# Optimization experiments

Measured on AMD Instinct MI355X. Metric: run time of the kernel, lower is better.

## Reference

```python
import jax, jax.numpy as jnp
import numpy as np

B, N, CIN, COUT, P = 16, 10000, 8, 32, 8
E = 160000
TRAIN_OR_PREDICT = 1


def setup_inputs() -> dict:
    key = jax.random.key(0)
    ks = jax.random.split(key, 12)
    inp = {}
    inp["X"] = jax.random.normal(ks[0], (B, N, CIN, 2 * P), dtype=jnp.float32)
    inp["edge_index"] = jax.random.randint(ks[1], (2, E), 0, N, dtype=jnp.int64)
    inp["edge_weight"] = jax.random.uniform(ks[2], (E,), dtype=jnp.float32)
    inp["attention"] = jax.random.uniform(ks[3], (2 * P,), dtype=jnp.float32)
    sc = 1.0 / np.sqrt(CIN)
    sl = 1.0 / np.sqrt(2 * COUT)
    names = ["z", "r", "h"]
    for i, g in enumerate(names):
        inp["Wc" + g] = jax.random.normal(ks[4 + i], (CIN, COUT), dtype=jnp.float32) * sc
        inp["bc" + g] = jnp.zeros((COUT,), dtype=jnp.float32)
        inp["Wl" + g] = jax.random.normal(ks[7 + i], (2 * COUT, COUT), dtype=jnp.float32) * sl
        inp["bl" + g] = jnp.zeros((COUT,), dtype=jnp.float32)
    return inp


def _gcn_norm(edge_index, edge_weight, n):
    # PyG gcn_norm: add self-loops (weight 1.0), symmetric D^-1/2 (A+I) D^-1/2
    src, dst = edge_index[0], edge_index[1]
    loop = jnp.arange(n)
    src = jnp.concatenate([src, loop])
    dst = jnp.concatenate([dst, loop])
    w = jnp.concatenate([edge_weight, jnp.ones((n,), edge_weight.dtype)])
    deg = jax.ops.segment_sum(w, dst, num_segments=n)
    dinv = jnp.where(deg > 0, deg ** -0.5, 0.0)
    return src, dst, dinv[src] * w * dinv[dst]


def _gcn(X, W, b, src, dst, norm, n):
    # propagate-then-transform: (A_hat X) W + b  (linear, identical to X W then A_hat)
    msg = X[:, src, :] * norm[None, :, None]                     # (B, E', Cin)
    agg = jax.ops.segment_sum(jnp.swapaxes(msg, 0, 1), dst, num_segments=n)  # (N, B, Cin)
    return jnp.einsum('bni,io->bno', jnp.swapaxes(agg, 0, 1), W) + b


def reference(X, edge_index, edge_weight, attention,
              Wcz, bcz, Wlz, blz, Wcr, bcr, Wlr, blr, Wch, bch, Wlh, blh):
    b_, n, _, t2 = X.shape
    p = t2 // 2
    src, dst, norm = _gcn_norm(edge_index, edge_weight, n)
    probs = jax.nn.softmax(attention)
    # backward half of the sum is scaled by TrainorPredict (linearity of the weighted sum)
    ws = jnp.concatenate([probs[:p], probs[p:] * TRAIN_OR_PREDICT])
    H0 = jnp.zeros((b_, n, Wlz.shape[1]), X.dtype)
    Xs = jnp.moveaxis(X, 3, 0)  # (2P, B, N, Cin); H is never chained in the original loop

    def cell(x):
        Z = jax.nn.sigmoid(jnp.concatenate([_gcn(x, Wcz, bcz, src, dst, norm, n), H0], -1) @ Wlz + blz)
        R = jax.nn.sigmoid(jnp.concatenate([_gcn(x, Wcr, bcr, src, dst, norm, n), H0], -1) @ Wlr + blr)
        Ht = jnp.tanh(jnp.concatenate([_gcn(x, Wch, bch, src, dst, norm, n), H0 * R], -1) @ Wlh + blh)
        return Z * H0 + (1.0 - Z) * Ht

    def step(acc, pw):
        x, w = pw
        return acc + w * cell(x), None

    out, _ = jax.lax.scan(step, H0, (Xs, ws))
    return out
```

## Files before the change

### kernel.cpp

```cpp
#include <hip/hip_runtime.h>
#include <stdint.h>

#define NN 10000
#define NE 160000
#define NB 16
#define NT 8

typedef __attribute__((ext_vector_type(8))) float f32x8;
typedef __attribute__((ext_vector_type(4))) float f32x4;
typedef __attribute__((ext_vector_type(2))) float f32x2;
typedef __attribute__((ext_vector_type(8))) _Float16 h16x8;

#define AGG_LD 136

__device__ __forceinline__ int ei_stride(const int* __restrict__ ei) {
    int z = ei[1] | ei[3] | ei[5] | ei[7] | ei[9] | ei[11] | ei[13] | ei[15];
    return (z == 0) ? 2 : 1;
}

__global__ void k_zero(float* deg, int* count) {
    int i = blockIdx.x * blockDim.x + threadIdx.x;
    if (i < NN) { deg[i] = 0.f; count[i] = 0; }
}

__global__ __launch_bounds__(256)
void k_repack(const float* __restrict__ X, h16x8* __restrict__ X2,
              float* dz, int* cz) {
    int gid = blockIdx.x * blockDim.x + threadIdx.x;
    int gsz = gridDim.x * blockDim.x;
    for (int i = gid; i < NN; i += gsz) { dz[i] = 0.f; cz[i] = 0; }
    const int total = NN * 256;
    for (int i = gid; i < total; i += gsz) {
        int n = i >> 8, t = i & 255;
        int b = t >> 4, chunk = t & 15;
        f32x8 w = ((const f32x8*)X)[((size_t)b * NN + n) * 16 + chunk];
        h16x8 h;
        #pragma unroll
        for (int j = 0; j < 8; ++j) h[j] = (_Float16)w[j];
        X2[((size_t)(b >> 1) * NN + n) * 32 + (b & 1) * 16 + chunk] = h;
    }
}

__global__ void k_degree(const int* __restrict__ ei, const float* __restrict__ ew,
                         float* deg, int* count) {
    int e = blockIdx.x * blockDim.x + threadIdx.x;
    if (e >= NE) return;
    int stride = ei_stride(ei);
    int d = ei[(size_t)(NE + e) * stride];
    atomicAdd(&deg[d], ew[e]);
    atomicAdd(&count[d], 1);
}

__global__ void k_scan_consts(const float* __restrict__ deg, const int* __restrict__ count,
                              float* dinv, int* offsets, int* fillptr,
                              const float* __restrict__ attn,
                              const float* __restrict__ Wcz, const float* __restrict__ bcz,
                              const float* __restrict__ Wlz, const float* __restrict__ blz,
                              const float* __restrict__ Wch, const float* __restrict__ bch,
                              const float* __restrict__ Wlh, const float* __restrict__ blh,
                              float* consts) {
    int tid = threadIdx.x;
    if (blockIdx.x == 1) {
        if (tid < 256) {
            int c = tid >> 5, o = tid & 31;
            float mz = 0.f, mh = 0.f;
            for (int k = 0; k < 32; ++k) {
                mz += Wcz[c * 32 + k] * Wlz[k * 32 + o];
                mh += Wch[c * 32 + k] * Wlh[k * 32 + o];
            }
            consts[tid] = mz;
            consts[256 + tid] = mh;
        }
        if (tid < 32) {
            float cz = blz[tid], ch = blh[tid];
            for (int k = 0; k < 32; ++k) {
                cz += bcz[k] * Wlz[k * 32 + tid];
                ch += bch[k] * Wlh[k * 32 + tid];
            }
            consts[512 + tid] = cz;
            consts[544 + tid] = ch;
        }
        if (tid == 0) {
            float a[16], m = -1e30f, s = 0.f;
            for (int t = 0; t < 16; ++t) { a[t] = attn[t]; m = fmaxf(m, a[t]); }
            for (int t = 0; t < 16; ++t) { a[t] = __expf(a[t] - m); s += a[t]; }
            for (int t = 0; t < 16; ++t) consts[576 + t] = a[t] / s;
        }
        return;
    }
    int lane = tid & 63, wv = tid >> 6;
    __shared__ int wsum[16];
    __shared__ int carry;
    if (tid == 0) carry = 0;
    __syncthreads();
    for (int base = 0; base < NN; base += 1024) {
        int i = base + tid;
        int v = (i < NN) ? count[i] : 0;
        int x = v;
        #pragma unroll
        for (int s = 1; s < 64; s <<= 1) {
            int y = __shfl_up(x, s, 64);
            if (lane >= s) x += y;
        }
        if (lane == 63) wsum[wv] = x;
        __syncthreads();
        if (wv == 0 && lane < 16) {
            int y = wsum[lane];
            #pragma unroll
            for (int s = 1; s < 16; s <<= 1) {
                int z = __shfl_up(y, s, 64);
                if (lane >= s) y += z;
            }
            wsum[lane] = y;
        }
        __syncthreads();
        int wbase = (wv == 0) ? 0 : wsum[wv - 1];
        int incl = carry + wbase + x;
        int excl = incl - v;
        if (i < NN) { offsets[i] = excl; fillptr[i] = excl; }
        __syncthreads();
        if (tid == 1023) carry = incl;
        __syncthreads();
    }
    for (int i = tid; i < NN; i += 1024) dinv[i] = rsqrtf(deg[i] + 1.0f);
}

__global__ void k_fill(const int* __restrict__ ei, const float* __restrict__ ew,
                       const float* __restrict__ dinv,
                       int* fillptr, int* csr_src, float* csr_norm) {
    int e = blockIdx.x * blockDim.x + threadIdx.x;
    if (e >= NE) return;
    int stride = ei_stride(ei);
    int s = ei[(size_t)e * stride];
    int d = ei[(size_t)(NE + e) * stride];
    int pos = atomicAdd(&fillptr[d], 1);
    csr_src[pos] = s;
    csr_norm[pos] = dinv[s] * ew[e] * dinv[d];
}

__device__ __forceinline__ float gatefn(float uz, float uh) {
    float ez = __expf(uz);
    float eh = __expf(2.f * uh);
    return (eh - 1.f) * __builtin_amdgcn_rcpf((1.f + ez) * (eh + 1.f));
}

__global__ __launch_bounds__(256)
void k_main_h(const h16x8* __restrict__ X2,
              const int* __restrict__ offsets, const int* __restrict__ count,
              const float* __restrict__ dinv,
              const int* __restrict__ csr_src, const float* __restrict__ csr_norm,
              const float* __restrict__ consts,
              float* __restrict__ out) {
    __shared__ float sAgg[2 * NT * AGG_LD];
    __shared__ float sMz[256], sMh[256], sCz[32], sCh[32], sWs[16];
    int tid = threadIdx.x;
    int bp   = blockIdx.x & 7;
    int tile = blockIdx.x >> 3;

    sMz[tid] = consts[tid];
    sMh[tid] = consts[256 + tid];
    if (tid < 32) { sCz[tid] = consts[512 + tid]; sCh[tid] = consts[544 + tid]; }
    if (tid < 16) sWs[tid] = consts[576 + tid];

    int ns = tid >> 5;
    int lane = tid & 31;
    int n = tile * NT + ns;
    const h16x8* xb = X2 + ((size_t)bp * NN) * 32;
    float dn = dinv[n];
    float selfn = dn * dn;
    float acc[8];
    {
        h16x8 w = xb[(size_t)n * 32 + lane];
        #pragma unroll
        for (int j = 0; j < 8; ++j) acc[j] = selfn * (float)w[j];
    }
    int off = offsets[n], cnt = count[n];
    const int*   sp  = csr_src + off;
    const float* npv = csr_norm + off;
    int e = 0;
    if (cnt >= 8) {
        int s0 = sp[0], s1 = sp[1], s2 = sp[2], s3 = sp[3];
        h16x8 a0 = xb[(size_t)s0 * 32 + lane];
        h16x8 a1 = xb[(size_t)s1 * 32 + lane];
        h16x8 a2 = xb[(size_t)s2 * 32 + lane];
        h16x8 a3 = xb[(size_t)s3 * 32 + lane];
        for (e = 4; e + 4 <= cnt; e += 4) {
            int t0 = sp[e], t1 = sp[e + 1], t2 = sp[e + 2], t3 = sp[e + 3];
            h16x8 b0 = xb[(size_t)t0 * 32 + lane];
            h16x8 b1 = xb[(size_t)t1 * 32 + lane];
            h16x8 b2 = xb[(size_t)t2 * 32 + lane];
            h16x8 b3 = xb[(size_t)t3 * 32 + lane];
            __builtin_amdgcn_sched_barrier(0);
            float n0 = npv[e - 4], n1 = npv[e - 3], n2 = npv[e - 2], n3 = npv[e - 1];
            #pragma unroll
            for (int j = 0; j < 8; ++j) acc[j] += n0 * (float)a0[j];
            #pragma unroll
            for (int j = 0; j < 8; ++j) acc[j] += n1 * (float)a1[j];
            #pragma unroll
            for (int j = 0; j < 8; ++j) acc[j] += n2 * (float)a2[j];
            #pragma unroll
            for (int j = 0; j < 8; ++j) acc[j] += n3 * (float)a3[j];
            a0 = b0; a1 = b1; a2 = b2; a3 = b3;
        }
        float n0 = npv[e - 4], n1 = npv[e - 3], n2 = npv[e - 2], n3 = npv[e - 1];
        #pragma unroll
        for (int j = 0; j < 8; ++j) acc[j] += n0 * (float)a0[j];
        #pragma unroll
        for (int j = 0; j < 8; ++j) acc[j] += n1 * (float)a1[j];
        #pragma unroll
        for (int j = 0; j < 8; ++j) acc[j] += n2 * (float)a2[j];
        #pragma unroll
        for (int j = 0; j < 8; ++j) acc[j] += n3 * (float)a3[j];
    }
    for (; e < cnt; ++e) {
        int s = sp[e];
        float nrm = npv[e];
        h16x8 w = xb[(size_t)s * 32 + lane];
        #pragma unroll
        for (int j = 0; j < 8; ++j) acc[j] += nrm * (float)w[j];
    }
    {
        int half = lane >> 4;
        int chunk = lane & 15;
        int r = ns * 2 + half;
        int c = chunk >> 1;
        int tpb = (chunk & 1) * 4;
        float* rowp = &sAgg[r * AGG_LD + c * 2];
        #pragma unroll
        for (int k = 0; k < 4; ++k) {
            f32x2 v = {acc[2 * k], acc[2 * k + 1]};
            *(f32x2*)&rowp[(tpb + k) * 16] = v;
        }
    }
    __syncthreads();

    int o = tid & 31, ns2 = tid >> 5;
    int n2 = tile * NT + ns2;
    float mz[8], mh[8];
    #pragma unroll
    for (int c = 0; c < 8; ++c) { mz[c] = sMz[c * 32 + o]; mh[c] = sMh[c * 32 + o]; }
    float czo = sCz[o], cho = sCh[o];
    const f32x4* r0 = (const f32x4*)&sAgg[(ns2 * 2 + 0) * AGG_LD];
    const f32x4* r1 = (const f32x4*)&sAgg[(ns2 * 2 + 1) * AGG_LD];
    f32x2 out0 = {0.f, 0.f}, out1 = {0.f, 0.f};
    #pragma unroll
    for (int tp = 0; tp < 8; ++tp) {
        f32x4 A0[4], A1[4];
        #pragma unroll
        for (int k = 0; k < 4; ++k) { A0[k] = r0[tp * 4 + k]; A1[k] = r1[tp * 4 + k]; }
        f32x2 uz0 = {czo, czo}, uh0 = {cho, cho};
        f32x2 uz1 = {czo, czo}, uh1 = {cho, cho};
        #pragma unroll
        for (int k = 0; k < 4; ++k) {
            f32x2 p0 = A0[k].xy, q0 = A0[k].zw;
            f32x2 p1 = A1[k].xy, q1 = A1[k].zw;
            float m0 = mz[2 * k], m1 = mz[2 * k + 1];
            float v0 = mh[2 * k], v1 = mh[2 * k + 1];
            uz0 += p0 * m0; uz0 += q0 * m1;
            uh0 += p0 * v0; uh0 += q0 * v1;
            uz1 += p1 * m0; uz1 += q1 * m1;
            uh1 += p1 * v0; uh1 += q1 * v1;
        }
        f32x2 wsp = {sWs[2 * tp], sWs[2 * tp + 1]};
        f32x2 g0, g1;
        g0.x = gatefn(uz0.x, uh0.x); g0.y = gatefn(uz0.y, uh0.y);
        g1.x = gatefn(uz1.x, uh1.x); g1.y = gatefn(uz1.y, uh1.y);
        out0 += wsp * g0;
        out1 += wsp * g1;
    }
    out[((size_t)(bp * 2 + 0) * NN + n2) * 32 + o] = out0.x + out0.y;
    out[((size_t)(bp * 2 + 1) * NN + n2) * 32 + o] = out1.x + out1.y;
}

__global__ __launch_bounds__(256)
void k_main_f32(const float* __restrict__ X,
                const int* __restrict__ offsets, const int* __restrict__ count,
                const float* __restrict__ dinv,
                const int* __restrict__ csr_src, const float* __restrict__ csr_norm,
                const float* __restrict__ consts,
                float* __restrict__ out) {
    __shared__ float sAgg[NB * 128];
    __shared__ float sMz[256], sMh[256], sCz[32], sCh[32], sWs[16];
    int tid = threadIdx.x;
    int n = blockIdx.x;

    sMz[tid] = consts[tid];
    sMh[tid] = consts[256 + tid];
    if (tid < 32) { sCz[tid] = consts[512 + tid]; sCh[tid] = consts[544 + tid]; }
    if (tid < 16) sWs[tid] = consts[576 + tid];

    int b = tid >> 4, chunk = tid & 15;
    const f32x8* xv = (const f32x8*)X;
    float dn = dinv[n];
    float selfn = dn * dn;
    float acc[8];
    {
        f32x8 w = xv[((size_t)b * NN + n) * 16 + chunk];
        #pragma unroll
        for (int j = 0; j < 8; ++j) acc[j] = selfn * w[j];
    }
    int off = offsets[n], cnt = count[n];
    for (int e = off; e < off + cnt; ++e) {
        int s = csr_src[e];
        float nrm = csr_norm[e];
        f32x8 w = xv[((size_t)b * NN + s) * 16 + chunk];
        #pragma unroll
        for (int j = 0; j < 8; ++j) acc[j] += nrm * w[j];
    }
    #pragma unroll
    for (int j = 0; j < 8; ++j) sAgg[tid * 8 + j] = acc[j];
    __syncthreads();

    int o = tid & 31, b0 = tid >> 5;
    float mz[8], mh[8];
    #pragma unroll
    for (int c = 0; c < 8; ++c) { mz[c] = sMz[c * 32 + o]; mh[c] = sMh[c * 32 + o]; }
    float czo = sCz[o], cho = sCh[o];
    float acc0 = 0.f, acc1 = 0.f;
    #pragma unroll
    for (int t = 0; t < 16; ++t) {
        float uz0 = czo, uh0 = cho, uz1 = czo, uh1 = cho;
        #pragma unroll
        for (int c = 0; c < 8; ++c) {
            float a0 = sAgg[b0 * 128 + c * 16 + t];
            float a1 = sAgg[(b0 + 8) * 128 + c * 16 + t];
            uz0 += a0 * mz[c]; uh0 += a0 * mh[c];
            uz1 += a1 * mz[c]; uh1 += a1 * mh[c];
        }
        float w = sWs[t];
        acc0 += w * gatefn(uz0, uh0);
        acc1 += w * gatefn(uz1, uh1);
    }
    out[((size_t)b0 * NN + n) * 32 + o]       = acc0;
    out[((size_t)(b0 + 8) * NN + n) * 32 + o] = acc1;
}

extern "C" void kernel_launch(void* const* d_in, const int* in_sizes, int n_in,
                              void* d_out, int out_size, void* d_ws, size_t ws_size,
                              hipStream_t stream) {
    const float* X    = (const float*)d_in[0];
    const int*   ei   = (const int*)d_in[1];
    const float* ew   = (const float*)d_in[2];
    const float* attn = (const float*)d_in[3];
    const float* Wcz  = (const float*)d_in[4];
    const float* bcz  = (const float*)d_in[5];
    const float* Wlz  = (const float*)d_in[6];
    const float* blz  = (const float*)d_in[7];
    const float* Wch  = (const float*)d_in[12];
    const float* bch  = (const float*)d_in[13];
    const float* Wlh  = (const float*)d_in[14];
    const float* blh  = (const float*)d_in[15];
    float* out = (float*)d_out;

    const size_t x2_bytes = (size_t)NN * 256 * 16;
    const size_t small_bytes = (size_t)NN * 4 * 5 + (size_t)NE * 4 * 2 + 592 * 4;
    bool use_h = (ws_size >= x2_bytes + small_bytes);

    char* p = (char*)d_ws;
    h16x8* X2 = nullptr;
    if (use_h) { X2 = (h16x8*)p; p += x2_bytes; }
    float* deg      = (float*)p; p += NN * 4;
    float* dinv     = (float*)p; p += NN * 4;
    int*   count    = (int*)p;   p += NN * 4;
    int*   offsets  = (int*)p;   p += NN * 4;
    int*   fillptr  = (int*)p;   p += NN * 4;
    int*   csr_src  = (int*)p;   p += NE * 4;
    float* csr_norm = (float*)p; p += NE * 4;
    float* consts   = (float*)p; p += 592 * 4;

    if (use_h) {
        hipLaunchKernelGGL(k_repack, dim3(1280), dim3(256), 0, stream, X, X2, deg, count);
    } else {
        hipLaunchKernelGGL(k_zero, dim3((NN + 255) / 256), dim3(256), 0, stream, deg, count);
    }
    hipLaunchKernelGGL(k_degree, dim3((NE + 255) / 256), dim3(256), 0, stream, ei, ew, deg, count);
    hipLaunchKernelGGL(k_scan_consts, dim3(2), dim3(1024), 0, stream,
                       deg, count, dinv, offsets, fillptr,
                       attn, Wcz, bcz, Wlz, blz, Wch, bch, Wlh, blh, consts);
    hipLaunchKernelGGL(k_fill, dim3((NE + 255) / 256), dim3(256), 0, stream,
                       ei, ew, dinv, fillptr, csr_src, csr_norm);
    if (use_h) {
        hipLaunchKernelGGL(k_main_h, dim3((NN / NT) * 8), dim3(256), 0, stream,
                           X2, offsets, count, dinv, csr_src, csr_norm, consts, out);
    } else {
        hipLaunchKernelGGL(k_main_f32, dim3(NN), dim3(256), 0, stream,
                           X, offsets, count, dinv, csr_src, csr_norm, consts, out);
    }
}
```

Baseline: 155.6 us.

## Fuse prep kernels and split each node's edges across half-waves

Merges the repack, degree-count and constant-folding kernels into one grid-stride prep kernel. A memset now zeroes deg and count, which were reordered to sit next to each other, and the scan runs as its own one-block kernel. The main kernel now uses NT=4 nodes per block with one 64-lane wave per node: each half-wave gathers alternate edges, and a shuffle-xor combines the two partial sums, which doubles memory-level parallelism per node and halves the per-thread gather count. The epilogue handles one (batch,node) row per 32 threads, and the grid doubles in block count with more per-block constant loading overhead.

```diff
diff --git a/kernel.cpp b/kernel.cpp
--- a/kernel.cpp
+++ b/kernel.cpp
@@ -4,7 +4,7 @@
 #define NN 10000
 #define NE 160000
 #define NB 16
-#define NT 8
+#define NT 4
 
 typedef __attribute__((ext_vector_type(8))) float f32x8;
 typedef __attribute__((ext_vector_type(4))) float f32x4;
@@ -18,50 +18,39 @@
     return (z == 0) ? 2 : 1;
 }
 
-__global__ void k_zero(float* deg, int* count) {
-    int i = blockIdx.x * blockDim.x + threadIdx.x;
-    if (i < NN) { deg[i] = 0.f; count[i] = 0; }
-}
-
 __global__ __launch_bounds__(256)
-void k_repack(const float* __restrict__ X, h16x8* __restrict__ X2,
-              float* dz, int* cz) {
+void k_prep(const float* __restrict__ X, h16x8* __restrict__ X2, int do_repack,
+            const int* __restrict__ ei, const float* __restrict__ ew,
+            float* deg, int* count,
+            const float* __restrict__ attn,
+            const float* __restrict__ Wcz, const float* __restrict__ bcz,
+            const float* __restrict__ Wlz, const float* __restrict__ blz,
+            const float* __restrict__ Wch, const float* __restrict__ bch,
+            const float* __restrict__ Wlh, const float* __restrict__ blh,
+            float* consts) {
     int gid = blockIdx.x * blockDim.x + threadIdx.x;
     int gsz = gridDim.x * blockDim.x;
-    for (int i = gid; i < NN; i += gsz) { dz[i] = 0.f; cz[i] = 0; }
-    const int total = NN * 256;
-    for (int i = gid; i < total; i += gsz) {
-        int n = i >> 8, t = i & 255;
-        int b = t >> 4, chunk = t & 15;
-        f32x8 w = ((const f32x8*)X)[((size_t)b * NN + n) * 16 + chunk];
-        h16x8 h;
-        #pragma unroll
-        for (int j = 0; j < 8; ++j) h[j] = (_Float16)w[j];
-        X2[((size_t)(b >> 1) * NN + n) * 32 + (b & 1) * 16 + chunk] = h;
-    }
-}
-
-__global__ void k_degree(const int* __restrict__ ei, const float* __restrict__ ew,
-                         float* deg, int* count) {
-    int e = blockIdx.x * blockDim.x + threadIdx.x;
-    if (e >= NE) return;
     int stride = ei_stride(ei);
-    int d = ei[(size_t)(NE + e) * stride];
-    atomicAdd(&deg[d], ew[e]);
-    atomicAdd(&count[d], 1);
-}
-
-__global__ void k_scan_consts(const float* __restrict__ deg, const int* __restrict__ count,
-                              float* dinv, int* offsets, int* fillptr,
-                              const float* __restrict__ attn,
-                              const float* __restrict__ Wcz, const float* __restrict__ bcz,
-                              const float* __restrict__ Wlz, const float* __restrict__ blz,
-                              const float* __restrict__ Wch, const float* __restrict__ bch,
-                              const float* __restrict__ Wlh, const float* __restrict__ blh,
-                              float* consts) {
-    int tid = threadIdx.x;
-    if (blockIdx.x == 1) {
-        if (tid < 256) {
+    for (int e = gid; e < NE; e += gsz) {
+        int d = ei[(size_t)(NE + e) * stride];
+        atomicAdd(&deg[d], ew[e]);
+        atomicAdd(&count[d], 1);
+    }
+    if (do_repack) {
+        const int total = NN * 256;
+        for (int i = gid; i < total; i += gsz) {
+            int n = i >> 8, t = i & 255;
+            int b = t >> 4, chunk = t & 15;
+            f32x8 w = ((const f32x8*)X)[((size_t)b * NN + n) * 16 + chunk];
+            h16x8 h;
+            #pragma unroll
+            for (int j = 0; j < 8; ++j) h[j] = (_Float16)w[j];
+            X2[((size_t)(b >> 1) * NN + n) * 32 + (b & 1) * 16 + chunk] = h;
+        }
+    }
+    if (blockIdx.x == 0) {
+        int tid = threadIdx.x;
+        {
             int c = tid >> 5, o = tid & 31;
             float mz = 0.f, mh = 0.f;
             for (int k = 0; k < 32; ++k) {
@@ -86,8 +75,12 @@
             for (int t = 0; t < 16; ++t) { a[t] = __expf(a[t] - m); s += a[t]; }
             for (int t = 0; t < 16; ++t) consts[576 + t] = a[t] / s;
         }
-        return;
-    }
+    }
+}
+
+__global__ void k_scan(const float* __restrict__ deg, const int* __restrict__ count,
+                       float* dinv, int* offsets, int* fillptr) {
+    int tid = threadIdx.x;
     int lane = tid & 63, wv = tid >> 6;
     __shared__ int wsum[16];
     __shared__ int carry;
@@ -162,15 +155,17 @@
     if (tid < 32) { sCz[tid] = consts[512 + tid]; sCh[tid] = consts[544 + tid]; }
     if (tid < 16) sWs[tid] = consts[576 + tid];
 
-    int ns = tid >> 5;
-    int lane = tid & 31;
-    int n = tile * NT + ns;
+    int lane = tid & 63;
+    int wv = __builtin_amdgcn_readfirstlane(tid >> 6);
+    int half = lane >> 5;
+    int chunk = lane & 31;
+    int n = tile * NT + wv;
     const h16x8* xb = X2 + ((size_t)bp * NN) * 32;
     float dn = dinv[n];
-    float selfn = dn * dn;
+    float selfn = (half == 0) ? dn * dn : 0.f;
     float acc[8];
     {
-        h16x8 w = xb[(size_t)n * 32 + lane];
+        h16x8 w = xb[(size_t)n * 32 + chunk];
         #pragma unroll
         for (int j = 0; j < 8; ++j) acc[j] = selfn * (float)w[j];
     }
@@ -180,51 +175,54 @@
     int e = 0;
     if (cnt >= 8) {
         int s0 = sp[0], s1 = sp[1], s2 = sp[2], s3 = sp[3];
-        h16x8 a0 = xb[(size_t)s0 * 32 + lane];
-        h16x8 a1 = xb[(size_t)s1 * 32 + lane];
-        h16x8 a2 = xb[(size_t)s2 * 32 + lane];
-        h16x8 a3 = xb[(size_t)s3 * 32 + lane];
+        int sa = half ? s1 : s0, sb = half ? s3 : s2;
+        h16x8 a0 = xb[(size_t)sa * 32 + chunk];
+        h16x8 a1 = xb[(size_t)sb * 32 + chunk];
         for (e = 4; e + 4 <= cnt; e += 4) {
             int t0 = sp[e], t1 = sp[e + 1], t2 = sp[e + 2], t3 = sp[e + 3];
-            h16x8 b0 = xb[(size_t)t0 * 32 + lane];
-            h16x8 b1 = xb[(size_t)t1 * 32 + lane];
-            h16x8 b2 = xb[(size_t)t2 * 32 + lane];
-            h16x8 b3 = xb[(size_t)t3 * 32 + lane];
+            int ta = half ? t1 : t0, tb = half ? t3 : t2;
+            h16x8 b0 = xb[(size_t)ta * 32 + chunk];
+            h16x8 b1 = xb[(size_t)tb * 32 + chunk];
             __builtin_amdgcn_sched_barrier(0);
             float n0 = npv[e - 4], n1 = npv[e - 3], n2 = npv[e - 2], n3 = npv[e - 1];
+            float na = half ? n1 : n0, nb = half ? n3 : n2;
             #pragma unroll
-            for (int j = 0; j < 8; ++j) acc[j] += n0 * (float)a0[j];
+            for (int j = 0; j < 8; ++j) acc[j] += na * (float)a0[j];
             #pragma unroll
-            for (int j = 0; j < 8; ++j) acc[j] += n1 * (float)a1[j];
-            #pragma unroll
-            for (int j = 0; j < 8; ++j) acc[j] += n2 * (float)a2[j];
-            #pragma unroll
-            for (int j = 0; j < 8; ++j) acc[j] += n3 * (float)a3[j];
-            a0 = b0; a1 = b1; a2 = b2; a3 = b3;
+            for (int j = 0; j < 8; ++j) acc[j] += nb * (float)a1[j];
+            a0 = b0; a1 = b1;
         }
         float n0 = npv[e - 4], n1 = npv[e - 3], n2 = npv[e - 2], n3 = npv[e - 1];
-        #pragma unroll
-        for (int j = 0; j < 8; ++j) acc[j] += n0 * (float)a0[j];
-        #pragma unroll
-        for (int j = 0; j < 8; ++j) acc[j] += n1 * (float)a1[j];
-        #pragma unroll
-        for (int j = 0; j < 8; ++j) acc[j] += n2 * (float)a2[j];
-        #pragma unroll
-        for (int j = 0; j < 8; ++j) acc[j] += n3 * (float)a3[j];
-    }
-    for (; e < cnt; ++e) {
+        float na = half ? n1 : n0, nb = half ? n3 : n2;
+        #pragma unroll
+        for (int j = 0; j < 8; ++j) acc[j] += na * (float)a0[j];
+        #pragma unroll
+        for (int j = 0; j < 8; ++j) acc[j] += nb * (float)a1[j];
+    }
+    for (; e + 2 <= cnt; e += 2) {
+        int s0 = sp[e], s1 = sp[e + 1];
+        int sa = half ? s1 : s0;
+        float n0 = npv[e], n1 = npv[e + 1];
+        float na = half ? n1 : n0;
+        h16x8 w = xb[(size_t)sa * 32 + chunk];
+        #pragma unroll
+        for (int j = 0; j < 8; ++j) acc[j] += na * (float)w[j];
+    }
+    if (e < cnt) {
         int s = sp[e];
-        float nrm = npv[e];
-        h16x8 w = xb[(size_t)s * 32 + lane];
+        float nrm = half ? 0.f : npv[e];
+        h16x8 w = xb[(size_t)s * 32 + chunk];
         #pragma unroll
         for (int j = 0; j < 8; ++j) acc[j] += nrm * (float)w[j];
     }
-    {
-        int half = lane >> 4;
-        int chunk = lane & 15;
-        int r = ns * 2 + half;
-        int c = chunk >> 1;
-        int tpb = (chunk & 1) * 4;
+    #pragma unroll
+    for (int j = 0; j < 8; ++j) acc[j] += __shfl_xor(acc[j], 32);
+    if (lane < 32) {
+        int bl = chunk >> 4;
+        int sub = chunk & 15;
+        int r = wv * 2 + bl;
+        int c = sub >> 1;
+        int tpb = (sub & 1) * 4;
         float* rowp = &sAgg[r * AGG_LD + c * 2];
         #pragma unroll
         for (int k = 0; k < 4; ++k) {
@@ -234,42 +232,34 @@
     }
     __syncthreads();
 
-    int o = tid & 31, ns2 = tid >> 5;
-    int n2 = tile * NT + ns2;
+    int o = tid & 31, rr = tid >> 5;
     float mz[8], mh[8];
     #pragma unroll
     for (int c = 0; c < 8; ++c) { mz[c] = sMz[c * 32 + o]; mh[c] = sMh[c * 32 + o]; }
     float czo = sCz[o], cho = sCh[o];
-    const f32x4* r0 = (const f32x4*)&sAgg[(ns2 * 2 + 0) * AGG_LD];
-    const f32x4* r1 = (const f32x4*)&sAgg[(ns2 * 2 + 1) * AGG_LD];
-    f32x2 out0 = {0.f, 0.f}, out1 = {0.f, 0.f};
+    const f32x4* r0 = (const f32x4*)&sAgg[rr * AGG_LD];
+    f32x2 o0 = {0.f, 0.f};
     #pragma unroll
     for (int tp = 0; tp < 8; ++tp) {
-        f32x4 A0[4], A1[4];
-        #pragma unroll
-        for (int k = 0; k < 4; ++k) { A0[k] = r0[tp * 4 + k]; A1[k] = r1[tp * 4 + k]; }
-        f32x2 uz0 = {czo, czo}, uh0 = {cho, cho};
-        f32x2 uz1 = {czo, czo}, uh1 = {cho, cho};
+        f32x4 A0[4];
+        #pragma unroll
+        for (int k = 0; k < 4; ++k) A0[k] = r0[tp * 4 + k];
+        f32x2 uz = {czo, czo}, uh = {cho, cho};
         #pragma unroll
         for (int k = 0; k < 4; ++k) {
-            f32x2 p0 = A0[k].xy, q0 = A0[k].zw;
-            f32x2 p1 = A1[k].xy, q1 = A1[k].zw;
-            float m0 = mz[2 * k], m1 = mz[2 * k + 1];
-            float v0 = mh[2 * k], v1 = mh[2 * k + 1];
-            uz0 += p0 * m0; uz0 += q0 * m1;
-            uh0 += p0 * v0; uh0 += q0 * v1;
-            uz1 += p1 * m0; uz1 += q1 * m1;
-            uh1 += p1 * v0; uh1 += q1 * v1;
+            f32x2 p = A0[k].xy, q = A0[k].zw;
+            uz += p * mz[2 * k]; uz += q * mz[2 * k + 1];
+            uh += p * mh[2 * k]; uh += q * mh[2 * k + 1];
         }
         f32x2 wsp = {sWs[2 * tp], sWs[2 * tp + 1]};
-        f32x2 g0, g1;
-        g0.x = gatefn(uz0.x, uh0.x); g0.y = gatefn(uz0.y, uh0.y);
-        g1.x = gatefn(uz1.x, uh1.x); g1.y = gatefn(uz1.y, uh1.y);
-        out0 += wsp * g0;
-        out1 += wsp * g1;
-    }
-    out[((size_t)(bp * 2 + 0) * NN + n2) * 32 + o] = out0.x + out0.y;
-    out[((size_t)(bp * 2 + 1) * NN + n2) * 32 + o] = out1.x + out1.y;
+        f32x2 g;
+        g.x = gatefn(uz.x, uh.x);
+        g.y = gatefn(uz.y, uh.y);
+        o0 += wsp * g;
+    }
+    int b  = bp * 2 + (rr & 1);
+    int n2 = tile * NT + (rr >> 1);
+    out[((size_t)b * NN + n2) * 32 + o] = o0.x + o0.y;
 }
 
 __global__ __launch_bounds__(256)
@@ -360,23 +350,20 @@
     h16x8* X2 = nullptr;
     if (use_h) { X2 = (h16x8*)p; p += x2_bytes; }
     float* deg      = (float*)p; p += NN * 4;
+    int*   count    = (int*)p;   p += NN * 4;
     float* dinv     = (float*)p; p += NN * 4;
-    int*   count    = (int*)p;   p += NN * 4;
     int*   offsets  = (int*)p;   p += NN * 4;
     int*   fillptr  = (int*)p;   p += NN * 4;
     int*   csr_src  = (int*)p;   p += NE * 4;
     float* csr_norm = (float*)p; p += NE * 4;
     float* consts   = (float*)p; p += 592 * 4;
 
-    if (use_h) {
-        hipLaunchKernelGGL(k_repack, dim3(1280), dim3(256), 0, stream, X, X2, deg, count);
-    } else {
-        hipLaunchKernelGGL(k_zero, dim3((NN + 255) / 256), dim3(256), 0, stream, deg, count);
-    }
-    hipLaunchKernelGGL(k_degree, dim3((NE + 255) / 256), dim3(256), 0, stream, ei, ew, deg, count);
-    hipLaunchKernelGGL(k_scan_consts, dim3(2), dim3(1024), 0, stream,
-                       deg, count, dinv, offsets, fillptr,
+    hipMemsetAsync(deg, 0, (size_t)NN * 8, stream);
+    hipLaunchKernelGGL(k_prep, dim3(1280), dim3(256), 0, stream,
+                       X, X2, use_h ? 1 : 0, ei, ew, deg, count,
                        attn, Wcz, bcz, Wlz, blz, Wch, bch, Wlh, blh, consts);
+    hipLaunchKernelGGL(k_scan, dim3(1), dim3(1024), 0, stream,
+                       deg, count, dinv, offsets, fillptr);
     hipLaunchKernelGGL(k_fill, dim3((NE + 255) / 256), dim3(256), 0, stream,
                        ei, ew, dinv, fillptr, csr_src, csr_norm);
     if (use_h) {
```

After: 154.0 us. About the same (-1.0%).
